# Optimization experiments

Measured on AMD Instinct MI355X. Metric: run time of the kernel, lower is better.

## Reference

```python
import jax, jax.numpy as jnp
import numpy as np

N = 8192
PERCEPTION = 0.2
SEP_DIST = 0.02
ACC_SCALE = 1.0
ACC_MAX = 1.0
EPS = 1e-08


def setup_inputs() -> dict:
    key = jax.random.key(0)
    k1, k2, k3 = jax.random.split(key, 3)
    position = jax.random.uniform(k1, (N, 2), dtype=jnp.float32)  # boids live in [0,1]^2 torus
    velocity = jax.random.normal(k2, (N, 2), dtype=jnp.float32) * 0.05
    noise = jax.random.uniform(k3, (N, 2), dtype=jnp.float32, minval=-1.0, maxval=1.0)
    return {
        "position": position,
        "velocity": velocity,
        "noise": noise,
        "separation_weight": jnp.float32(4.5),
        "alignment_weight": jnp.float32(0.65),
        "cohesion_weight": jnp.float32(0.75),
        "noise_scale": jnp.float32(0.05),
    }


def _normalize(v):
    # per-row normalize, matching module's _normalize
    norm = jnp.maximum(jnp.linalg.norm(v, axis=-1, keepdims=True), EPS)
    return v / norm


def reference(position, velocity, noise, separation_weight, alignment_weight, cohesion_weight, noise_scale):
    # Toroidal vector from boid i to boid j: diff[i, j, :]  (shape [N, N, 2])
    diff = position[None, :, :] - position[:, None, :]
    diff = jnp.where(diff > 0.5, diff - 1.0, diff)
    diff = jnp.where(diff < -0.5, diff + 1.0, diff)
    dist2 = jnp.sum(diff * diff, axis=-1)  # [N, N]

    not_self = ~jnp.eye(N, dtype=bool)

    # Separation: sum of -toroidal_vector over too-close neighbors, normalized
    sep_mask = not_self & (dist2 <= SEP_DIST ** 2)
    steer_sep = -jnp.sum(jnp.where(sep_mask[..., None], diff, 0.0), axis=1)
    steer_sep = _normalize(steer_sep)

    # Perception mask shared by alignment and cohesion
    perc_mask = not_self & (dist2 <= PERCEPTION ** 2)
    cnt = jnp.sum(perc_mask, axis=1, dtype=position.dtype)[:, None]  # [N, 1]

    # Alignment: mean neighbor velocity minus own velocity, normalized
    vel_avg = jnp.einsum("ij,jd->id", perc_mask.astype(position.dtype), velocity) / cnt
    steer_align = _normalize(vel_avg - velocity)

    # Cohesion: mean toroidal vector to neighbors, normalized
    pos_avg = jnp.sum(jnp.where(perc_mask[..., None], diff, 0.0), axis=1) / cnt
    steer_coh = _normalize(pos_avg)

    acc = (separation_weight * steer_sep
           + alignment_weight * steer_align
           + cohesion_weight * steer_coh)
    acc = acc * ACC_SCALE
    acc = acc + noise_scale * noise

    # clip by norm per boid
    norm = jnp.linalg.norm(acc, axis=-1, keepdims=True)
    acc = jnp.where(norm > ACC_MAX, acc * ACC_MAX / jnp.maximum(norm, EPS), acc)
    return acc
```

## Files before the change

kernel.cpp:

```cpp
#include <hip/hip_runtime.h>
#include <math.h>

#define N_BOIDS 8192
typedef float f32x2 __attribute__((ext_vector_type(2)));
typedef float f32x4 __attribute__((ext_vector_type(4)));

constexpr int   NC     = 16;
constexpr int   NCELL  = NC * NC;
constexpr float MARG   = 0.2002f;
constexpr int   CHUNK  = 256;
constexpr int   NBLK   = N_BOIDS / CHUNK;
constexpr size_t HIST_OFF = 0;
constexpr size_t BASE_OFF = 32768;
constexpr size_t CS_OFF   = 65536;
constexpr size_t SORT_OFF = 69632;
constexpr size_t SIDX_OFF = 200704;
constexpr size_t WS_NEED  = 233472;

constexpr float SEP_R2  = 4.0000000000000008e-04f;
constexpr float PERC_R2 = 4.0000000000000001e-02f;
constexpr float EPSF    = 1e-08f;

__device__ __forceinline__ int cell_of(float px, float py) {
    int cx = (int)(px * 16.0f); cx = cx > 15 ? 15 : (cx < 0 ? 0 : cx);
    int cy = (int)(py * 16.0f); cy = cy > 15 ? 15 : (cy < 0 ? 0 : cy);
    return cy * NC + cx;
}

__global__ __launch_bounds__(CHUNK) void cell_hist(
    const float* __restrict__ pos, int* __restrict__ hist)
{
    __shared__ int h[NCELL];
    const int tid = threadIdx.x;
    h[tid] = 0;
    __syncthreads();
    const int i = blockIdx.x * CHUNK + tid;
    atomicAdd(&h[cell_of(pos[2 * i], pos[2 * i + 1])], 1);
    __syncthreads();
    hist[blockIdx.x * NCELL + tid] = h[tid];
}

__global__ __launch_bounds__(NCELL) void cell_scan(
    const int* __restrict__ hist, int* __restrict__ base, int* __restrict__ cs)
{
    __shared__ int tot[NCELL];
    __shared__ int sc[NCELL + 1];
    const int c = threadIdx.x;
    int hh[NBLK];
    int t = 0;
#pragma unroll
    for (int b = 0; b < NBLK; ++b) { hh[b] = hist[b * NCELL + c]; t += hh[b]; }
    tot[c] = t;
    __syncthreads();
    if (c == 0) {
        int run = 0;
        for (int k = 0; k < NCELL; ++k) { sc[k] = run; run += tot[k]; }
        sc[NCELL] = run;
    }
    __syncthreads();
    cs[c] = sc[c];
    if (c == 0) cs[NCELL] = sc[NCELL];
    int run2 = sc[c];
#pragma unroll
    for (int b = 0; b < NBLK; ++b) { base[b * NCELL + c] = run2; run2 += hh[b]; }
}

__global__ __launch_bounds__(CHUNK) void cell_scatter(
    const float* __restrict__ pos, const float* __restrict__ vel,
    const int* __restrict__ base, float4* __restrict__ sorted4,
    int* __restrict__ sidx)
{
    __shared__ int cid[CHUNK];
    __shared__ int lbase[NCELL];
    const int tid = threadIdx.x;
    const int b   = blockIdx.x;
    const int i   = b * CHUNK + tid;
    const float px = pos[2 * i], py = pos[2 * i + 1];
    const int c = cell_of(px, py);
    cid[tid]   = c;
    lbase[tid] = base[b * NCELL + tid];
    __syncthreads();
    int rank = 0;
    for (int t2 = 0; t2 < tid; ++t2) rank += (cid[t2] == c) ? 1 : 0;
    const int slot = lbase[c] + rank;
    float4 o; o.x = px; o.y = py; o.z = vel[2 * i]; o.w = vel[2 * i + 1];
    sorted4[slot] = o;
    sidx[slot]    = i;
}

__device__ __forceinline__ void finalize_core(
    float vix, float viy, const f32x2 nz,
    float ws, float wa, float wc, float wn,
    float sx, float sy, float vx, float vy, float cx, float cy, float cntall,
    float* __restrict__ out, int orig)
{
    const float cnt = cntall - 1.0f;
    float ns  = fmaxf(sqrtf(sx * sx + sy * sy), EPSF);
    float ssx = sx / ns, ssy = sy / ns;
    float vax = (vx - vix) / cnt - vix;
    float vay = (vy - viy) / cnt - viy;
    float na  = fmaxf(sqrtf(vax * vax + vay * vay), EPSF);
    float sax = vax / na, say = vay / na;
    float pax = cx / cnt, pay = cy / cnt;
    float nc  = fmaxf(sqrtf(pax * pax + pay * pay), EPSF);
    float scx = pax / nc, scy = pay / nc;
    float ax = ws * ssx + wa * sax + wc * scx;
    float ay = ws * ssy + wa * say + wc * scy;
    ax += wn * nz.x;
    ay += wn * nz.y;
    const float nn = sqrtf(ax * ax + ay * ay);
    if (nn > 1.0f) {
        const float s = 1.0f / fmaxf(nn, EPSF);
        ax *= s;
        ay *= s;
    }
    out[2 * orig]     = ax;
    out[2 * orig + 1] = ay;
}

__global__ __launch_bounds__(256, 4) void boids_main(
    const float4* __restrict__ sorted4,
    const int* __restrict__ sidx,
    const int* __restrict__ cs,
    const f32x2* __restrict__ noise,
    const float* __restrict__ w_sep,
    const float* __restrict__ w_ali,
    const float* __restrict__ w_coh,
    const float* __restrict__ w_noise,
    float* __restrict__ out)
{
    __shared__ int cs_l[NCELL + 1];
    const int tid = threadIdx.x;
    cs_l[tid] = cs[tid];
    if (tid == 0) cs_l[NCELL] = cs[NCELL];
    __syncthreads();

    const int lane = tid & 63;
    const int wid  = tid >> 6;
    const int i0   = (blockIdx.x * 4 + wid) * 2;

    const float4 I0 = sorted4[i0];
    const float4 I1 = sorted4[i0 + 1];
    const float vperc = PERC_R2;
    const float vsep  = SEP_R2;

    const float xmn = fminf(I0.x, I1.x), xmx = fmaxf(I0.x, I1.x);
    const float ymn = fminf(I0.y, I1.y), ymx = fmaxf(I0.y, I1.y);
    const int cx0 = (int)floorf((xmn - MARG) * 16.0f);
    const int cx1 = (int)floorf((xmx + MARG) * 16.0f);
    const int cy0 = (int)floorf((ymn - MARG) * 16.0f);
    const int cy1 = (int)floorf((ymx + MARG) * 16.0f);
    int nx = cx1 - cx0 + 1; if (nx > NC) nx = NC;
    int ny = cy1 - cy0 + 1; if (ny > NC) ny = NC;

    float n0 = 0.f, s0x = 0.f, s0y = 0.f, v0x = 0.f, v0y = 0.f, c0x = 0.f, c0y = 0.f;
    float n1 = 0.f, s1x = 0.f, s1y = 0.f, v1x = 0.f, v1y = 0.f, c1x = 0.f, c1y = 0.f;

    for (int r = 0; r < ny; ++r) {
        const int ry      = (cy0 + r) & (NC - 1);
        const int rowbase = ry * NC;
        const int a0      = cx0 & (NC - 1);
        const int lenA    = (nx < NC - a0) ? nx : (NC - a0);
        const int lenB    = nx - lenA;
        const int sA = cs_l[rowbase + a0];
        const int eA = cs_l[rowbase + a0 + lenA];
        const int sB = cs_l[rowbase];
        const int eB = cs_l[rowbase + lenB];
        for (int seg = 0; seg < 2; ++seg) {
            const int js = seg ? sB : sA;
            const int je = seg ? eB : eA;
            for (int j0 = js; j0 < je; j0 += 64) {
                const int   rem = je - j0;
                const int   jj  = (lane < rem) ? (j0 + lane) : j0;
                const float inv = (lane < rem) ? 0.0f : 1e9f;
                const float4 q  = sorted4[jj];
                float dx0, dy0, dx1, dy1, ta, tb, tc, m;
                asm(
                    "v_sub_f32   %[dx0], %[qx], %[p0x]\n\t"
                    "v_sub_f32   %[dy0], %[qy], %[p0y]\n\t"
                    "v_sub_f32   %[dx1], %[qx], %[p1x]\n\t"
                    "v_sub_f32   %[dy1], %[qy], %[p1y]\n\t"
                    "v_rndne_f32 %[ta], %[dx0]\n\t"
                    "v_rndne_f32 %[tb], %[dy0]\n\t"
                    "v_sub_f32   %[dx0], %[dx0], %[ta]\n\t"
                    "v_sub_f32   %[dy0], %[dy0], %[tb]\n\t"
                    "v_rndne_f32 %[ta], %[dx1]\n\t"
                    "v_rndne_f32 %[tb], %[dy1]\n\t"
                    "v_sub_f32   %[dx1], %[dx1], %[ta]\n\t"
                    "v_sub_f32   %[dy1], %[dy1], %[tb]\n\t"
                    "v_mul_f32   %[ta], %[dx0], %[dx0]\n\t"
                    "v_mul_f32   %[tb], %[dy0], %[dy0]\n\t"
                    "v_add_f32   %[ta], %[ta], %[tb]\n\t"
                    "v_max_f32   %[ta], %[ta], %[inv]\n\t"
                    "v_mul_f32   %[tb], %[dx1], %[dx1]\n\t"
                    "v_mul_f32   %[tc], %[dy1], %[dy1]\n\t"
                    "v_add_f32   %[tb], %[tb], %[tc]\n\t"
                    "v_max_f32   %[tb], %[tb], %[inv]\n\t"
                    "v_cmp_ge_f32 vcc, %[vperc], %[ta]\n\t"
                    "v_cndmask_b32 %[m], 0, 1.0, vcc\n\t"
                    "v_add_f32   %[n0], %[n0], %[m]\n\t"
                    "v_fmac_f32  %[v0x], %[m], %[qz]\n\t"
                    "v_fmac_f32  %[v0y], %[m], %[qw]\n\t"
                    "v_fmac_f32  %[c0x], %[m], %[dx0]\n\t"
                    "v_fmac_f32  %[c0y], %[m], %[dy0]\n\t"
                    "v_cmp_ge_f32 vcc, %[vperc], %[tb]\n\t"
                    "v_cndmask_b32 %[m], 0, 1.0, vcc\n\t"
                    "v_add_f32   %[n1], %[n1], %[m]\n\t"
                    "v_fmac_f32  %[v1x], %[m], %[qz]\n\t"
                    "v_fmac_f32  %[v1y], %[m], %[qw]\n\t"
                    "v_fmac_f32  %[c1x], %[m], %[dx1]\n\t"
                    "v_fmac_f32  %[c1y], %[m], %[dy1]\n\t"
                    "v_cmp_ge_f32 vcc, %[vsep], %[ta]\n\t"
                    "v_cndmask_b32 %[m], 0, 1.0, vcc\n\t"
                    "v_fma_f32   %[s0x], -%[m], %[dx0], %[s0x]\n\t"
                    "v_fma_f32   %[s0y], -%[m], %[dy0], %[s0y]\n\t"
                    "v_cmp_ge_f32 vcc, %[vsep], %[tb]\n\t"
                    "v_cndmask_b32 %[m], 0, 1.0, vcc\n\t"
                    "v_fma_f32   %[s1x], -%[m], %[dx1], %[s1x]\n\t"
                    "v_fma_f32   %[s1y], -%[m], %[dy1], %[s1y]\n\t"
                    : [dx0] "=&v"(dx0), [dy0] "=&v"(dy0),
                      [dx1] "=&v"(dx1), [dy1] "=&v"(dy1),
                      [ta] "=&v"(ta), [tb] "=&v"(tb), [tc] "=&v"(tc), [m] "=&v"(m),
                      [n0] "+v"(n0), [s0x] "+v"(s0x), [s0y] "+v"(s0y),
                      [v0x] "+v"(v0x), [v0y] "+v"(v0y),
                      [c0x] "+v"(c0x), [c0y] "+v"(c0y),
                      [n1] "+v"(n1), [s1x] "+v"(s1x), [s1y] "+v"(s1y),
                      [v1x] "+v"(v1x), [v1y] "+v"(v1y),
                      [c1x] "+v"(c1x), [c1y] "+v"(c1y)
                    : [qx] "v"(q.x), [qy] "v"(q.y), [qz] "v"(q.z), [qw] "v"(q.w),
                      [p0x] "v"(I0.x), [p0y] "v"(I0.y),
                      [p1x] "v"(I1.x), [p1y] "v"(I1.y),
                      [vperc] "v"(vperc), [vsep] "v"(vsep), [inv] "v"(inv)
                    : "vcc");
            }
        }
    }

#pragma unroll
    for (int mlev = 1; mlev < 64; mlev <<= 1) {
        n0  += __shfl_xor(n0,  mlev);
        s0x += __shfl_xor(s0x, mlev);  s0y += __shfl_xor(s0y, mlev);
        v0x += __shfl_xor(v0x, mlev);  v0y += __shfl_xor(v0y, mlev);
        c0x += __shfl_xor(c0x, mlev);  c0y += __shfl_xor(c0y, mlev);
        n1  += __shfl_xor(n1,  mlev);
        s1x += __shfl_xor(s1x, mlev);  s1y += __shfl_xor(s1y, mlev);
        v1x += __shfl_xor(v1x, mlev);  v1y += __shfl_xor(v1y, mlev);
        c1x += __shfl_xor(c1x, mlev);  c1y += __shfl_xor(c1y, mlev);
    }

    if (lane < 2) {
        float sx = s0x, sy = s0y, vx = v0x, vy = v0y, cx = c0x, cy = c0y, cc = n0;
        float vix = I0.z, viy = I0.w;
        if (lane == 1) {
            sx = s1x; sy = s1y; vx = v1x; vy = v1y; cx = c1x; cy = c1y; cc = n1;
            vix = I1.z; viy = I1.w;
        }
        const int orig = sidx[i0 + lane];
        finalize_core(vix, viy, noise[orig],
                      w_sep[0], w_ali[0], w_coh[0], w_noise[0],
                      sx, sy, vx, vy, cx, cy, cc, out, orig);
    }
}

constexpr int FB_BLOCK = 256;
constexpr int FB_TILE  = 2048;

__global__ __launch_bounds__(FB_BLOCK, 4) void boids_allpairs(
    const f32x2* __restrict__ pos, const f32x2* __restrict__ vel,
    const f32x2* __restrict__ noise,
    const float* __restrict__ w_sep, const float* __restrict__ w_ali,
    const float* __restrict__ w_coh, const float* __restrict__ w_noise,
    float* __restrict__ out)
{
    __shared__ f32x4 tile[FB_TILE];
    const int tid  = threadIdx.x;
    const int lane = tid & 63;
    const int wid  = tid >> 6;
    const int i0   = (blockIdx.x * 4 + wid) * 2;
    const f32x2 P0 = pos[i0];
    const f32x2 P1 = pos[i0 + 1];
    const float vperc = PERC_R2, vsep = SEP_R2;
    float n0 = 0.f, s0x = 0.f, s0y = 0.f, v0x = 0.f, v0y = 0.f, c0x = 0.f, c0y = 0.f;
    float n1 = 0.f, s1x = 0.f, s1y = 0.f, v1x = 0.f, v1y = 0.f, c1x = 0.f, c1y = 0.f;
    for (int t = 0; t < N_BOIDS / FB_TILE; ++t) {
        const f32x4* gp = reinterpret_cast<const f32x4*>(pos) + t * (FB_TILE / 2);
        const f32x4* gv = reinterpret_cast<const f32x4*>(vel) + t * (FB_TILE / 2);
#pragma unroll
        for (int c = 0; c < FB_TILE / 2 / FB_BLOCK; ++c) {
            const int idx  = tid + c * FB_BLOCK;
            const f32x4 pp = gp[idx];
            const f32x4 vv = gv[idx];
            f32x4 t0; t0.x = pp.x; t0.y = pp.y; t0.z = vv.x; t0.w = vv.y;
            f32x4 t1; t1.x = pp.z; t1.y = pp.w; t1.z = vv.z; t1.w = vv.w;
            tile[2 * idx] = t0; tile[2 * idx + 1] = t1;
        }
        __syncthreads();
#pragma unroll 8
        for (int k = 0; k < FB_TILE / 64; ++k) {
            const f32x4 q = tile[lane + k * 64];
            float dx, dy, ta, tb, m;
            asm("v_sub_f32 %[dx], %[qx], %[p0x]\n\t"
                "v_sub_f32 %[dy], %[qy], %[p0y]\n\t"
                "v_rndne_f32 %[ta], %[dx]\n\t"
                "v_rndne_f32 %[tb], %[dy]\n\t"
                "v_sub_f32 %[dx], %[dx], %[ta]\n\t"
                "v_sub_f32 %[dy], %[dy], %[tb]\n\t"
                "v_mul_f32 %[ta], %[dx], %[dx]\n\t"
                "v_mul_f32 %[tb], %[dy], %[dy]\n\t"
                "v_add_f32 %[ta], %[ta], %[tb]\n\t"
                "v_cmp_ge_f32 vcc, %[vperc], %[ta]\n\t"
                "v_cndmask_b32 %[m], 0, 1.0, vcc\n\t"
                "v_add_f32 %[n0], %[n0], %[m]\n\t"
                "v_fmac_f32 %[v0x], %[m], %[qz]\n\t"
                "v_fmac_f32 %[v0y], %[m], %[qw]\n\t"
                "v_fmac_f32 %[c0x], %[m], %[dx]\n\t"
                "v_fmac_f32 %[c0y], %[m], %[dy]\n\t"
                "v_cmp_ge_f32 vcc, %[vsep], %[ta]\n\t"
                "v_cndmask_b32 %[m], 0, 1.0, vcc\n\t"
                "v_fma_f32 %[s0x], -%[m], %[dx], %[s0x]\n\t"
                "v_fma_f32 %[s0y], -%[m], %[dy], %[s0y]\n\t"
                "v_sub_f32 %[dx], %[qx], %[p1x]\n\t"
                "v_sub_f32 %[dy], %[qy], %[p1y]\n\t"
                "v_rndne_f32 %[ta], %[dx]\n\t"
                "v_rndne_f32 %[tb], %[dy]\n\t"
                "v_sub_f32 %[dx], %[dx], %[ta]\n\t"
                "v_sub_f32 %[dy], %[dy], %[tb]\n\t"
                "v_mul_f32 %[ta], %[dx], %[dx]\n\t"
                "v_mul_f32 %[tb], %[dy], %[dy]\n\t"
                "v_add_f32 %[ta], %[ta], %[tb]\n\t"
                "v_cmp_ge_f32 vcc, %[vperc], %[ta]\n\t"
                "v_cndmask_b32 %[m], 0, 1.0, vcc\n\t"
                "v_add_f32 %[n1], %[n1], %[m]\n\t"
                "v_fmac_f32 %[v1x], %[m], %[qz]\n\t"
                "v_fmac_f32 %[v1y], %[m], %[qw]\n\t"
                "v_fmac_f32 %[c1x], %[m], %[dx]\n\t"
                "v_fmac_f32 %[c1y], %[m], %[dy]\n\t"
                "v_cmp_ge_f32 vcc, %[vsep], %[ta]\n\t"
                "v_cndmask_b32 %[m], 0, 1.0, vcc\n\t"
                "v_fma_f32 %[s1x], -%[m], %[dx], %[s1x]\n\t"
                "v_fma_f32 %[s1y], -%[m], %[dy], %[s1y]\n\t"
                : [dx] "=&v"(dx), [dy] "=&v"(dy), [ta] "=&v"(ta),
                  [tb] "=&v"(tb), [m] "=&v"(m),
                  [n0] "+v"(n0), [s0x] "+v"(s0x), [s0y] "+v"(s0y),
                  [v0x] "+v"(v0x), [v0y] "+v"(v0y), [c0x] "+v"(c0x), [c0y] "+v"(c0y),
                  [n1] "+v"(n1), [s1x] "+v"(s1x), [s1y] "+v"(s1y),
                  [v1x] "+v"(v1x), [v1y] "+v"(v1y), [c1x] "+v"(c1x), [c1y] "+v"(c1y)
                : [qx] "v"(q.x), [qy] "v"(q.y), [qz] "v"(q.z), [qw] "v"(q.w),
                  [p0x] "v"(P0.x), [p0y] "v"(P0.y),
                  [p1x] "v"(P1.x), [p1y] "v"(P1.y),
                  [vperc] "v"(vperc), [vsep] "v"(vsep)
                : "vcc");
        }
        __syncthreads();
    }
#pragma unroll
    for (int mlev = 1; mlev < 64; mlev <<= 1) {
        n0  += __shfl_xor(n0,  mlev);
        s0x += __shfl_xor(s0x, mlev);  s0y += __shfl_xor(s0y, mlev);
        v0x += __shfl_xor(v0x, mlev);  v0y += __shfl_xor(v0y, mlev);
        c0x += __shfl_xor(c0x, mlev);  c0y += __shfl_xor(c0y, mlev);
        n1  += __shfl_xor(n1,  mlev);
        s1x += __shfl_xor(s1x, mlev);  s1y += __shfl_xor(s1y, mlev);
        v1x += __shfl_xor(v1x, mlev);  v1y += __shfl_xor(v1y, mlev);
        c1x += __shfl_xor(c1x, mlev);  c1y += __shfl_xor(c1y, mlev);
    }
    if (lane < 2) {
        float sx = s0x, sy = s0y, vx = v0x, vy = v0y, cx = c0x, cy = c0y, cc = n0;
        int i = i0;
        if (lane == 1) {
            sx = s1x; sy = s1y; vx = v1x; vy = v1y; cx = c1x; cy = c1y; cc = n1;
            i = i0 + 1;
        }
        finalize_core(vel[i].x, vel[i].y, noise[i],
                      w_sep[0], w_ali[0], w_coh[0], w_noise[0],
                      sx, sy, vx, vy, cx, cy, cc, out, i);
    }
}

extern "C" void kernel_launch(void* const* d_in, const int* in_sizes, int n_in,
                              void* d_out, int out_size, void* d_ws, size_t ws_size,
                              hipStream_t stream) {
    const float* pos_f   = (const float*)d_in[0];
    const float* vel_f   = (const float*)d_in[1];
    const f32x2* noise   = (const f32x2*)d_in[2];
    const float* w_sep   = (const float*)d_in[3];
    const float* w_ali   = (const float*)d_in[4];
    const float* w_coh   = (const float*)d_in[5];
    const float* w_noise = (const float*)d_in[6];
    float* out = (float*)d_out;

    if (ws_size >= WS_NEED) {
        char* wsb = (char*)d_ws;
        int*    hist    = (int*)(wsb + HIST_OFF);
        int*    base    = (int*)(wsb + BASE_OFF);
        int*    cs      = (int*)(wsb + CS_OFF);
        float4* sorted4 = (float4*)(wsb + SORT_OFF);
        int*    sidx    = (int*)(wsb + SIDX_OFF);
        cell_hist<<<NBLK, CHUNK, 0, stream>>>(pos_f, hist);
        cell_scan<<<1, NCELL, 0, stream>>>(hist, base, cs);
        cell_scatter<<<NBLK, CHUNK, 0, stream>>>(pos_f, vel_f, base, sorted4, sidx);
        boids_main<<<N_BOIDS / 8, 256, 0, stream>>>(
            sorted4, sidx, cs, noise, w_sep, w_ali, w_coh, w_noise, out);
    } else {
        boids_allpairs<<<N_BOIDS / 8, FB_BLOCK, 0, stream>>>(
            (const f32x2*)pos_f, (const f32x2*)vel_f, noise,
            w_sep, w_ali, w_coh, w_noise, out);
    }
}
```

Measured before the change: 41.13 us.

## Fuse cell scan into scatter and process one boid per wave

```diff
diff --git a/kernel.cpp b/kernel.cpp
--- a/kernel.cpp
+++ b/kernel.cpp
@@ -11,11 +11,10 @@
 constexpr int   CHUNK  = 256;
 constexpr int   NBLK   = N_BOIDS / CHUNK;
 constexpr size_t HIST_OFF = 0;
-constexpr size_t BASE_OFF = 32768;
-constexpr size_t CS_OFF   = 65536;
-constexpr size_t SORT_OFF = 69632;
-constexpr size_t SIDX_OFF = 200704;
-constexpr size_t WS_NEED  = 233472;
+constexpr size_t CS_OFF   = 32768;
+constexpr size_t SORT_OFF = 36864;
+constexpr size_t SIDX_OFF = 167936;
+constexpr size_t WS_NEED  = 200704;
 
 constexpr float SEP_R2  = 4.0000000000000008e-04f;
 constexpr float PERC_R2 = 4.0000000000000001e-02f;
@@ -40,49 +39,48 @@
     hist[blockIdx.x * NCELL + tid] = h[tid];
 }
 
-__global__ __launch_bounds__(NCELL) void cell_scan(
-    const int* __restrict__ hist, int* __restrict__ base, int* __restrict__ cs)
+__global__ __launch_bounds__(CHUNK) void cell_scan_scatter(
+    const float* __restrict__ pos, const float* __restrict__ vel,
+    const int* __restrict__ hist, int* __restrict__ cs,
+    float4* __restrict__ sorted4, int* __restrict__ sidx)
 {
     __shared__ int tot[NCELL];
-    __shared__ int sc[NCELL + 1];
+    __shared__ int lbase[NCELL];
+    __shared__ int cid[CHUNK];
     const int c = threadIdx.x;
-    int hh[NBLK];
-    int t = 0;
-#pragma unroll
-    for (int b = 0; b < NBLK; ++b) { hh[b] = hist[b * NCELL + c]; t += hh[b]; }
+    const int b = blockIdx.x;
+
+    int t = 0, part = 0;
+#pragma unroll
+    for (int bb = 0; bb < NBLK; ++bb) {
+        const int hv = hist[bb * NCELL + c];
+        t += hv;
+        if (bb < b) part += hv;
+    }
+    const int mytot = t;
     tot[c] = t;
     __syncthreads();
-    if (c == 0) {
-        int run = 0;
-        for (int k = 0; k < NCELL; ++k) { sc[k] = run; run += tot[k]; }
-        sc[NCELL] = run;
-    }
-    __syncthreads();
-    cs[c] = sc[c];
-    if (c == 0) cs[NCELL] = sc[NCELL];
-    int run2 = sc[c];
-#pragma unroll
-    for (int b = 0; b < NBLK; ++b) { base[b * NCELL + c] = run2; run2 += hh[b]; }
-}
-
-__global__ __launch_bounds__(CHUNK) void cell_scatter(
-    const float* __restrict__ pos, const float* __restrict__ vel,
-    const int* __restrict__ base, float4* __restrict__ sorted4,
-    int* __restrict__ sidx)
-{
-    __shared__ int cid[CHUNK];
-    __shared__ int lbase[NCELL];
-    const int tid = threadIdx.x;
-    const int b   = blockIdx.x;
-    const int i   = b * CHUNK + tid;
+#pragma unroll
+    for (int off = 1; off < NCELL; off <<= 1) {
+        int v = 0;
+        if (c >= off) v = tot[c - off];
+        __syncthreads();
+        tot[c] += v;
+        __syncthreads();
+    }
+    const int excl = tot[c] - mytot;
+    lbase[c] = excl + part;
+    cs[c] = excl;
+    if (c == NCELL - 1) cs[NCELL] = tot[NCELL - 1];
+
+    const int i = b * CHUNK + c;
     const float px = pos[2 * i], py = pos[2 * i + 1];
-    const int c = cell_of(px, py);
-    cid[tid]   = c;
-    lbase[tid] = base[b * NCELL + tid];
+    const int myc = cell_of(px, py);
+    cid[c] = myc;
     __syncthreads();
     int rank = 0;
-    for (int t2 = 0; t2 < tid; ++t2) rank += (cid[t2] == c) ? 1 : 0;
-    const int slot = lbase[c] + rank;
+    for (int t2 = 0; t2 < c; ++t2) rank += (cid[t2] == myc) ? 1 : 0;
+    const int slot = lbase[myc] + rank;
     float4 o; o.x = px; o.y = py; o.z = vel[2 * i]; o.w = vel[2 * i + 1];
     sorted4[slot] = o;
     sidx[slot]    = i;
@@ -118,7 +116,7 @@
     out[2 * orig + 1] = ay;
 }
 
-__global__ __launch_bounds__(256, 4) void boids_main(
+__global__ __launch_bounds__(256, 8) void boids_main(
     const float4* __restrict__ sorted4,
     const int* __restrict__ sidx,
     const int* __restrict__ cs,
@@ -137,31 +135,27 @@
 
     const int lane = tid & 63;
     const int wid  = tid >> 6;
-    const int i0   = (blockIdx.x * 4 + wid) * 2;
-
-    const float4 I0 = sorted4[i0];
-    const float4 I1 = sorted4[i0 + 1];
+    const int si   = blockIdx.x * 4 + wid;
+
+    const float4 I0 = sorted4[si];
     const float vperc = PERC_R2;
     const float vsep  = SEP_R2;
 
-    const float xmn = fminf(I0.x, I1.x), xmx = fmaxf(I0.x, I1.x);
-    const float ymn = fminf(I0.y, I1.y), ymx = fmaxf(I0.y, I1.y);
-    const int cx0 = (int)floorf((xmn - MARG) * 16.0f);
-    const int cx1 = (int)floorf((xmx + MARG) * 16.0f);
-    const int cy0 = (int)floorf((ymn - MARG) * 16.0f);
-    const int cy1 = (int)floorf((ymx + MARG) * 16.0f);
+    const int cx0 = (int)floorf((I0.x - MARG) * 16.0f);
+    const int cx1 = (int)floorf((I0.x + MARG) * 16.0f);
+    const int cy0 = (int)floorf((I0.y - MARG) * 16.0f);
+    const int cy1 = (int)floorf((I0.y + MARG) * 16.0f);
     int nx = cx1 - cx0 + 1; if (nx > NC) nx = NC;
     int ny = cy1 - cy0 + 1; if (ny > NC) ny = NC;
+    const int a0 = cx0 & (NC - 1);
+    const int lenA = (nx < NC - a0) ? nx : (NC - a0);
+    const int lenB = nx - lenA;
 
     float n0 = 0.f, s0x = 0.f, s0y = 0.f, v0x = 0.f, v0y = 0.f, c0x = 0.f, c0y = 0.f;
-    float n1 = 0.f, s1x = 0.f, s1y = 0.f, v1x = 0.f, v1y = 0.f, c1x = 0.f, c1y = 0.f;
 
     for (int r = 0; r < ny; ++r) {
         const int ry      = (cy0 + r) & (NC - 1);
         const int rowbase = ry * NC;
-        const int a0      = cx0 & (NC - 1);
-        const int lenA    = (nx < NC - a0) ? nx : (NC - a0);
-        const int lenB    = nx - lenA;
         const int sA = cs_l[rowbase + a0];
         const int eA = cs_l[rowbase + a0 + lenA];
         const int sB = cs_l[rowbase];
@@ -174,62 +168,36 @@
                 const int   jj  = (lane < rem) ? (j0 + lane) : j0;
                 const float inv = (lane < rem) ? 0.0f : 1e9f;
                 const float4 q  = sorted4[jj];
-                float dx0, dy0, dx1, dy1, ta, tb, tc, m;
+                float dx, dy, ta, tb, m;
                 asm(
-                    "v_sub_f32   %[dx0], %[qx], %[p0x]\n\t"
-                    "v_sub_f32   %[dy0], %[qy], %[p0y]\n\t"
-                    "v_sub_f32   %[dx1], %[qx], %[p1x]\n\t"
-                    "v_sub_f32   %[dy1], %[qy], %[p1y]\n\t"
-                    "v_rndne_f32 %[ta], %[dx0]\n\t"
-                    "v_rndne_f32 %[tb], %[dy0]\n\t"
-                    "v_sub_f32   %[dx0], %[dx0], %[ta]\n\t"
-                    "v_sub_f32   %[dy0], %[dy0], %[tb]\n\t"
-                    "v_rndne_f32 %[ta], %[dx1]\n\t"
-                    "v_rndne_f32 %[tb], %[dy1]\n\t"
-                    "v_sub_f32   %[dx1], %[dx1], %[ta]\n\t"
-                    "v_sub_f32   %[dy1], %[dy1], %[tb]\n\t"
-                    "v_mul_f32   %[ta], %[dx0], %[dx0]\n\t"
-                    "v_mul_f32   %[tb], %[dy0], %[dy0]\n\t"
+                    "v_sub_f32   %[dx], %[qx], %[px]\n\t"
+                    "v_sub_f32   %[dy], %[qy], %[py]\n\t"
+                    "v_rndne_f32 %[ta], %[dx]\n\t"
+                    "v_rndne_f32 %[tb], %[dy]\n\t"
+                    "v_sub_f32   %[dx], %[dx], %[ta]\n\t"
+                    "v_sub_f32   %[dy], %[dy], %[tb]\n\t"
+                    "v_mul_f32   %[ta], %[dx], %[dx]\n\t"
+                    "v_mul_f32   %[tb], %[dy], %[dy]\n\t"
                     "v_add_f32   %[ta], %[ta], %[tb]\n\t"
                     "v_max_f32   %[ta], %[ta], %[inv]\n\t"
-                    "v_mul_f32   %[tb], %[dx1], %[dx1]\n\t"
-                    "v_mul_f32   %[tc], %[dy1], %[dy1]\n\t"
-                    "v_add_f32   %[tb], %[tb], %[tc]\n\t"
-                    "v_max_f32   %[tb], %[tb], %[inv]\n\t"
                     "v_cmp_ge_f32 vcc, %[vperc], %[ta]\n\t"
                     "v_cndmask_b32 %[m], 0, 1.0, vcc\n\t"
                     "v_add_f32   %[n0], %[n0], %[m]\n\t"
                     "v_fmac_f32  %[v0x], %[m], %[qz]\n\t"
                     "v_fmac_f32  %[v0y], %[m], %[qw]\n\t"
-                    "v_fmac_f32  %[c0x], %[m], %[dx0]\n\t"
-                    "v_fmac_f32  %[c0y], %[m], %[dy0]\n\t"
-                    "v_cmp_ge_f32 vcc, %[vperc], %[tb]\n\t"
-                    "v_cndmask_b32 %[m], 0, 1.0, vcc\n\t"
-                    "v_add_f32   %[n1], %[n1], %[m]\n\t"
-                    "v_fmac_f32  %[v1x], %[m], %[qz]\n\t"
-                    "v_fmac_f32  %[v1y], %[m], %[qw]\n\t"
-                    "v_fmac_f32  %[c1x], %[m], %[dx1]\n\t"
-                    "v_fmac_f32  %[c1y], %[m], %[dy1]\n\t"
+                    "v_fmac_f32  %[c0x], %[m], %[dx]\n\t"
+                    "v_fmac_f32  %[c0y], %[m], %[dy]\n\t"
                     "v_cmp_ge_f32 vcc, %[vsep], %[ta]\n\t"
                     "v_cndmask_b32 %[m], 0, 1.0, vcc\n\t"
-                    "v_fma_f32   %[s0x], -%[m], %[dx0], %[s0x]\n\t"
-                    "v_fma_f32   %[s0y], -%[m], %[dy0], %[s0y]\n\t"
-                    "v_cmp_ge_f32 vcc, %[vsep], %[tb]\n\t"
-                    "v_cndmask_b32 %[m], 0, 1.0, vcc\n\t"
-                    "v_fma_f32   %[s1x], -%[m], %[dx1], %[s1x]\n\t"
-                    "v_fma_f32   %[s1y], -%[m], %[dy1], %[s1y]\n\t"
-                    : [dx0] "=&v"(dx0), [dy0] "=&v"(dy0),
-                      [dx1] "=&v"(dx1), [dy1] "=&v"(dy1),
-                      [ta] "=&v"(ta), [tb] "=&v"(tb), [tc] "=&v"(tc), [m] "=&v"(m),
+                    "v_fma_f32   %[s0x], -%[m], %[dx], %[s0x]\n\t"
+                    "v_fma_f32   %[s0y], -%[m], %[dy], %[s0y]\n\t"
+                    : [dx] "=&v"(dx), [dy] "=&v"(dy), [ta] "=&v"(ta),
+                      [tb] "=&v"(tb), [m] "=&v"(m),
                       [n0] "+v"(n0), [s0x] "+v"(s0x), [s0y] "+v"(s0y),
                       [v0x] "+v"(v0x), [v0y] "+v"(v0y),
-                      [c0x] "+v"(c0x), [c0y] "+v"(c0y),
-                      [n1] "+v"(n1), [s1x] "+v"(s1x), [s1y] "+v"(s1y),
-                      [v1x] "+v"(v1x), [v1y] "+v"(v1y),
-                      [c1x] "+v"(c1x), [c1y] "+v"(c1y)
+                      [c0x] "+v"(c0x), [c0y] "+v"(c0y)
                     : [qx] "v"(q.x), [qy] "v"(q.y), [qz] "v"(q.z), [qw] "v"(q.w),
-                      [p0x] "v"(I0.x), [p0y] "v"(I0.y),
-                      [p1x] "v"(I1.x), [p1y] "v"(I1.y),
+                      [px] "v"(I0.x), [py] "v"(I0.y),
                       [vperc] "v"(vperc), [vsep] "v"(vsep), [inv] "v"(inv)
                     : "vcc");
             }
@@ -242,23 +210,13 @@
         s0x += __shfl_xor(s0x, mlev);  s0y += __shfl_xor(s0y, mlev);
         v0x += __shfl_xor(v0x, mlev);  v0y += __shfl_xor(v0y, mlev);
         c0x += __shfl_xor(c0x, mlev);  c0y += __shfl_xor(c0y, mlev);
-        n1  += __shfl_xor(n1,  mlev);
-        s1x += __shfl_xor(s1x, mlev);  s1y += __shfl_xor(s1y, mlev);
-        v1x += __shfl_xor(v1x, mlev);  v1y += __shfl_xor(v1y, mlev);
-        c1x += __shfl_xor(c1x, mlev);  c1y += __shfl_xor(c1y, mlev);
-    }
-
-    if (lane < 2) {
-        float sx = s0x, sy = s0y, vx = v0x, vy = v0y, cx = c0x, cy = c0y, cc = n0;
-        float vix = I0.z, viy = I0.w;
-        if (lane == 1) {
-            sx = s1x; sy = s1y; vx = v1x; vy = v1y; cx = c1x; cy = c1y; cc = n1;
-            vix = I1.z; viy = I1.w;
-        }
-        const int orig = sidx[i0 + lane];
-        finalize_core(vix, viy, noise[orig],
+    }
+
+    if (lane == 0) {
+        const int orig = sidx[si];
+        finalize_core(I0.z, I0.w, noise[orig],
                       w_sep[0], w_ali[0], w_coh[0], w_noise[0],
-                      sx, sy, vx, vy, cx, cy, cc, out, orig);
+                      s0x, s0y, v0x, v0y, c0x, c0y, n0, out, orig);
     }
 }
 
@@ -392,14 +350,13 @@
     if (ws_size >= WS_NEED) {
         char* wsb = (char*)d_ws;
         int*    hist    = (int*)(wsb + HIST_OFF);
-        int*    base    = (int*)(wsb + BASE_OFF);
         int*    cs      = (int*)(wsb + CS_OFF);
         float4* sorted4 = (float4*)(wsb + SORT_OFF);
         int*    sidx    = (int*)(wsb + SIDX_OFF);
         cell_hist<<<NBLK, CHUNK, 0, stream>>>(pos_f, hist);
-        cell_scan<<<1, NCELL, 0, stream>>>(hist, base, cs);
-        cell_scatter<<<NBLK, CHUNK, 0, stream>>>(pos_f, vel_f, base, sorted4, sidx);
-        boids_main<<<N_BOIDS / 8, 256, 0, stream>>>(
+        cell_scan_scatter<<<NBLK, CHUNK, 0, stream>>>(pos_f, vel_f, hist, cs,
+                                                      sorted4, sidx);
+        boids_main<<<N_BOIDS / 4, 256, 0, stream>>>(
             sorted4, sidx, cs, noise, w_sep, w_ali, w_coh, w_noise, out);
     } else {
         boids_allpairs<<<N_BOIDS / 8, FB_BLOCK, 0, stream>>>(
```

Result: faster. 35.83 us (-12.9%).
